# Performance work log

Hardware: AMD Instinct MI355X
Metric: run time of the kernel (lower is better)

Reference implementation:

```python
import jax, jax.numpy as jnp
import numpy as np

B, T, C = 8, 2048, 256
H = 4
HD = C // H  # 64

def setup_inputs() -> dict:
    key = jax.random.key(0)
    ks = jax.random.split(key, 5)
    s = 1.0 / np.sqrt(C)
    return {
        "x": jax.random.normal(ks[0], (B, T, C), dtype=jnp.float32),
        "w_qkv": jax.random.uniform(ks[1], (3 * C, C), jnp.float32, -s, s),
        "b_qkv": jax.random.uniform(ks[2], (3 * C,), jnp.float32, -s, s),
        "w_proj": jax.random.uniform(ks[3], (C, C), jnp.float32, -s, s),
        "b_proj": jax.random.uniform(ks[4], (C,), jnp.float32, -s, s),
    }

def reference(x, w_qkv, b_qkv, w_proj, b_proj):
    # qkv projection: [B,T,3C] -> [3,B,H,T,HD]
    qkv = x @ w_qkv.T + b_qkv
    qkv = qkv.reshape(B, T, 3, H, HD).transpose(2, 0, 3, 1, 4)
    q, k, v = qkv[0], qkv[1], qkv[2]
    scale = HD ** -0.5
    attn = jnp.einsum("bhqd,bhkd->bhqk", q, k) * scale
    attn = jax.nn.softmax(attn, axis=-1)  # dropout is identity in eval
    out = jnp.einsum("bhqk,bhkd->bhqd", attn, v)
    out = out.transpose(0, 2, 1, 3).reshape(B, T, C)
    return out @ w_proj.T + b_proj
```

## Files before the change

### kernel.cpp

```cpp
#include <hip/hip_runtime.h>
#include <hip/hip_bf16.h>
#include <cstdint>
#include <cstddef>


typedef __attribute__((ext_vector_type(8))) __bf16 bf16x8;
typedef __attribute__((ext_vector_type(4))) float f32x4;
typedef __attribute__((ext_vector_type(16))) float f32x16;

__device__ __forceinline__ f32x4 mfma16(bf16x8 a, bf16x8 b, f32x4 c) {
  return __builtin_amdgcn_mfma_f32_16x16x32_bf16(a, b, c, 0, 0, 0);
}
__device__ __forceinline__ f32x16 mfma32(bf16x8 a, bf16x8 b, f32x16 c) {
  return __builtin_amdgcn_mfma_f32_32x32x16_bf16(a, b, c, 0, 0, 0);
}

__device__ __forceinline__ void gload_lds16(const __bf16* g, __bf16* l) {
  __builtin_amdgcn_global_load_lds(
      (const __attribute__((address_space(1))) void*)g,
      (__attribute__((address_space(3))) void*)l, 16, 0, 0);
}

__device__ __forceinline__ uint32_t cvtpk_bf16(float lo, float hi) {
  uint32_t r;
  asm("v_cvt_pk_bf16_f32 %0, %1, %2" : "=v"(r) : "v"(lo), "v"(hi));
  return r;
}

__global__ __launch_bounds__(256) void cast_all(
    const float* __restrict__ x, const float* __restrict__ wq,
    const float* __restrict__ wp,
    __bf16* __restrict__ xb, __bf16* __restrict__ wqb, __bf16* __restrict__ wpb) {
  const int NX = (16384 * 256) / 4, NQ = (768 * 256) / 4, NP = (256 * 256) / 4;
  int i = blockIdx.x * 256 + threadIdx.x;
  const float4* src;
  __bf16* dst;
  int j;
  if (i < NX) { src = (const float4*)x; dst = xb; j = i; }
  else if (i < NX + NQ) { src = (const float4*)wq; dst = wqb; j = i - NX; }
  else if (i < NX + NQ + NP) { src = (const float4*)wp; dst = wpb; j = i - NX - NQ; }
  else return;
  float4 v = src[j];
  union { __bf16 b[4]; ushort4 u; } o;
  o.b[0] = (__bf16)v.x; o.b[1] = (__bf16)v.y; o.b[2] = (__bf16)v.z; o.b[3] = (__bf16)v.w;
  ((ushort4*)dst)[j] = o.u;
}

template <int EPI>
__global__ __launch_bounds__(256) void gemm_nt(
    const __bf16* __restrict__ A, const __bf16* __restrict__ B,
    const float* __restrict__ bias, int K, int N,
    __bf16* __restrict__ qo, __bf16* __restrict__ ko, __bf16* __restrict__ vo,
    float* __restrict__ fo) {
  const int tid = threadIdx.x;
  const int lane = tid & 63;
  const int w = tid >> 6;
  const int wr = w >> 1, wc = w & 1;
  const int m0 = blockIdx.x * 128, n0 = blockIdx.y * 128;
  const int l15 = lane & 15, lhi = lane >> 4;
  const bool vswap = (EPI == 0) && (n0 >= 512);

  __shared__ __align__(16) __bf16 As[128 * 64];
  __shared__ __align__(16) __bf16 Bs[128 * 64];

  const f32x4 fzero = {0.f, 0.f, 0.f, 0.f};
  f32x4 acc[4][4];
#pragma unroll
  for (int i = 0; i < 4; i++)
#pragma unroll
    for (int j = 0; j < 4; j++) acc[i][j] = fzero;

  for (int k0 = 0; k0 < K; k0 += 64) {
#pragma unroll
    for (int it = 0; it < 4; ++it) {
      int c = it * 256 + tid;
      int row = c >> 3, cc = c & 7;
      int col = ((cc ^ (row & 7)) << 3);
      gload_lds16(A + (size_t)(m0 + row) * K + k0 + col, As + c * 8);
      gload_lds16(B + (size_t)(n0 + row) * K + k0 + col, Bs + c * 8);
    }
    asm volatile("s_waitcnt vmcnt(0)" ::: "memory");
    __syncthreads();

    bf16x8 af[4][2], bfr[4][2];
#pragma unroll
    for (int i = 0; i < 4; i++)
#pragma unroll
      for (int kk = 0; kk < 2; kk++) {
        af[i][kk]  = *(const bf16x8*)(
            As + (wr * 64 + i * 16 + l15) * 64 + (((kk * 4 + lhi) ^ (l15 & 7)) << 3));
        bfr[i][kk] = *(const bf16x8*)(
            Bs + (wc * 64 + i * 16 + l15) * 64 + (((kk * 4 + lhi) ^ (l15 & 7)) << 3));
      }
    __builtin_amdgcn_s_setprio(1);
    if (!vswap) {
#pragma unroll
      for (int kk = 0; kk < 2; kk++)
#pragma unroll
        for (int mi = 0; mi < 4; mi++)
#pragma unroll
          for (int ni = 0; ni < 4; ni++)
            acc[mi][ni] = mfma16(af[mi][kk], bfr[ni][kk], acc[mi][ni]);
    } else {
#pragma unroll
      for (int kk = 0; kk < 2; kk++)
#pragma unroll
        for (int mi = 0; mi < 4; mi++)
#pragma unroll
          for (int ni = 0; ni < 4; ni++)
            acc[mi][ni] = mfma16(bfr[ni][kk], af[mi][kk], acc[mi][ni]);
    }
    __builtin_amdgcn_s_setprio(0);
    __syncthreads();
  }

  if (vswap) {
#pragma unroll
    for (int mi = 0; mi < 4; mi++) {
#pragma unroll
      for (int ni = 0; ni < 4; ni++) {
        int tg = m0 + wr * 64 + mi * 16 + l15;
        int nb = n0 + wc * 64 + ni * 16 + (lhi << 2);
        int b = tg >> 11, t = tg & 2047;
#pragma unroll
        for (int r = 0; r < 4; r++) {
          int n = nb + r;
          float val = acc[mi][ni][r] + bias[n];
          int hd = n - 512;
          int h = hd >> 6, d = hd & 63;
          vo[((size_t)(b * 4 + h) * 64 + d) * 2048 + t] = (__bf16)val;
        }
      }
    }
    return;
  }

#pragma unroll
  for (int mi = 0; mi < 4; mi++) {
#pragma unroll
    for (int ni = 0; ni < 4; ni++) {
      int col = n0 + wc * 64 + ni * 16 + l15;
      int rowb = m0 + wr * 64 + mi * 16 + (lhi << 2);
      float bv = bias[col];
#pragma unroll
      for (int r = 0; r < 4; r++) {
        float val = acc[mi][ni][r] + bv;
        int rr = rowb + r;
        if (EPI == 0) {
          int h = (col >> 6) & 3;
          int d = col & 63;
          int b = rr >> 11;
          int t = rr & 2047;
          size_t bh = (size_t)(b * 4 + h);
          if (col < 256) {
            qo[(bh * 2048 + t) * 64 + d] = (__bf16)(val * 0.18033688f);
          } else {
            ko[(bh * 2048 + t) * 64 + d] = (__bf16)val;
          }
        } else {
          fo[(size_t)rr * N + col] = val;
        }
      }
    }
  }
}

__global__ __launch_bounds__(256, 2) void attn_kernel(
    const __bf16* __restrict__ Q, const __bf16* __restrict__ Kb,
    const __bf16* __restrict__ Vt, __bf16* __restrict__ Ao) {
  const int tid = threadIdx.x, lane = tid & 63, w = tid >> 6;
  const int l31 = lane & 31, hi = lane >> 5;
  const int bh = blockIdx.y;
  const int q0 = blockIdx.x * 128;
  const int b = bh >> 2, h = bh & 3;

  __shared__ __align__(16) __bf16 Ks[2][64 * 64];
  __shared__ __align__(16) __bf16 Vs[2][64 * 64];
  __shared__ float Ls[4][32];

  const __bf16* Qb = Q + (size_t)bh * 2048 * 64;
  const __bf16* Kbase = Kb + (size_t)bh * 2048 * 64;
  const __bf16* Vbase = Vt + (size_t)bh * 64 * 2048;

  const int qrow = q0 + w * 32 + l31;
  bf16x8 qf[4];
#pragma unroll
  for (int dc = 0; dc < 4; dc++)
    qf[dc] = *(const bf16x8*)(Qb + (size_t)qrow * 64 + dc * 16 + hi * 8);

  f32x16 oacc[2];
#pragma unroll
  for (int i = 0; i < 16; i++) { oacc[0][i] = 0.f; oacc[1][i] = 0.f; }
  float lrun = 0.f;

  const int r0 = tid >> 3, p0c = tid & 7;
  const int s0 = ((p0c ^ (r0 & 7)) << 3);
  const int r1 = (tid + 256) >> 3, p1c = tid & 7;
  const int s1 = ((p1c ^ (r1 & 7)) << 3);

  gload_lds16(Kbase + (size_t)r0 * 64 + s0, &Ks[0][tid * 8]);
  gload_lds16(Kbase + (size_t)r1 * 64 + s1, &Ks[0][(tid + 256) * 8]);
  gload_lds16(Vbase + (size_t)r0 * 2048 + s0, &Vs[0][tid * 8]);
  gload_lds16(Vbase + (size_t)r1 * 2048 + s1, &Vs[0][(tid + 256) * 8]);

  int cur = 0;
  const int swz = (l31 & 7);

  for (int kt = 0; kt < 32; ++kt) {
    __syncthreads();

    if (kt + 1 < 32) {
      const __bf16* Kg = Kbase + (size_t)(kt + 1) * 64 * 64;
      const __bf16* Vg = Vbase + (size_t)(kt + 1) * 64;
      gload_lds16(Kg + (size_t)r0 * 64 + s0, &Ks[cur ^ 1][tid * 8]);
      gload_lds16(Kg + (size_t)r1 * 64 + s1, &Ks[cur ^ 1][(tid + 256) * 8]);
      gload_lds16(Vg + (size_t)r0 * 2048 + s0, &Vs[cur ^ 1][tid * 8]);
      gload_lds16(Vg + (size_t)r1 * 2048 + s1, &Vs[cur ^ 1][(tid + 256) * 8]);
    }

    const __bf16* Kl = &Ks[cur][0];
    const __bf16* Vl = &Vs[cur][0];

    f32x16 sacc[2];
#pragma unroll
    for (int i = 0; i < 16; i++) { sacc[0][i] = -16.f; sacc[1][i] = -16.f; }
#pragma unroll
    for (int kb = 0; kb < 2; kb++) {
      bf16x8 kf[4];
#pragma unroll
      for (int dc = 0; dc < 4; dc++)
        kf[dc] = *(const bf16x8*)(
            Kl + (kb * 32 + l31) * 64 + (((dc * 2 + hi) ^ swz) << 3));
      __builtin_amdgcn_s_setprio(1);
#pragma unroll
      for (int dc = 0; dc < 4; dc++)
        sacc[kb] = mfma32(kf[dc], qf[dc], sacc[kb]);
      __builtin_amdgcn_s_setprio(0);
    }

#pragma unroll
    for (int kb = 0; kb < 2; kb++)
#pragma unroll
      for (int i = 0; i < 16; i++) sacc[kb][i] = exp2f(sacc[kb][i]);

    uint32_t wo[8][2];
#pragma unroll
    for (int kb = 0; kb < 2; kb++)
#pragma unroll
      for (int e = 0; e < 4; e++) {
        wo[kb * 4 + e][0] = cvtpk_bf16(sacc[kb][4 * e + 0], sacc[kb][4 * e + 1]);
        wo[kb * 4 + e][1] = cvtpk_bf16(sacc[kb][4 * e + 2], sacc[kb][4 * e + 3]);
      }
    bf16x8 pa[4];
#pragma unroll
    for (int ks = 0; ks < 4; ks++) {
      uint32_t a0 = wo[2 * ks][0], b0 = wo[2 * ks + 1][0];
      uint32_t a1 = wo[2 * ks][1], b1 = wo[2 * ks + 1][1];
      asm("v_permlane32_swap_b32 %0, %1" : "+v"(a0), "+v"(b0));
      asm("v_permlane32_swap_b32 %0, %1" : "+v"(a1), "+v"(b1));
      union { uint32_t u[4]; bf16x8 v; } f;
      f.u[0] = a0; f.u[1] = a1; f.u[2] = b0; f.u[3] = b1;
      pa[ks] = f.v;
    }

    float red[16];
#pragma unroll
    for (int i = 0; i < 16; i++) red[i] = sacc[0][i] + sacc[1][i];
#pragma unroll
    for (int s = 8; s >= 1; s >>= 1)
#pragma unroll
      for (int i = 0; i < 8; i++)
        if (i < s) red[i] += red[i + s];
    lrun += red[0] + __shfl_xor(red[0], 32);

#pragma unroll
    for (int db = 0; db < 2; db++) {
      bf16x8 vf[4];
#pragma unroll
      for (int ks = 0; ks < 4; ks++)
        vf[ks] = *(const bf16x8*)(
            Vl + (db * 32 + l31) * 64 + (((ks * 2 + hi) ^ swz) << 3));
      __builtin_amdgcn_s_setprio(1);
#pragma unroll
      for (int ks = 0; ks < 4; ks++)
        oacc[db] = mfma32(pa[ks], vf[ks], oacc[db]);
      __builtin_amdgcn_s_setprio(0);
    }

    cur ^= 1;
  }

  if (hi == 0) Ls[w][l31] = lrun;
  asm volatile("s_waitcnt lgkmcnt(0)" ::: "memory");
  __builtin_amdgcn_sched_barrier(0);
  float linv[16];
#pragma unroll
  for (int r = 0; r < 16; r++)
    linv[r] = 1.0f / Ls[w][4 * hi + (r & 3) + 8 * (r >> 2)];
#pragma unroll
  for (int db = 0; db < 2; db++)
#pragma unroll
    for (int r = 0; r < 16; r++) {
      int qr = 4 * hi + (r & 3) + 8 * (r >> 2);
      int t = q0 + w * 32 + qr;
      Ao[((size_t)(b * 2048 + t)) * 256 + h * 64 + db * 32 + l31] =
          (__bf16)(oacc[db][r] * linv[r]);
    }
}

extern "C" void kernel_launch(void* const* d_in, const int* in_sizes, int n_in,
                              void* d_out, int out_size, void* d_ws, size_t ws_size,
                              hipStream_t stream) {
  const float* x      = (const float*)d_in[0];
  const float* w_qkv  = (const float*)d_in[1];
  const float* b_qkv  = (const float*)d_in[2];
  const float* w_proj = (const float*)d_in[3];
  const float* b_proj = (const float*)d_in[4];
  float* out = (float*)d_out;

  char* ws = (char*)d_ws;
  __bf16* xb  = (__bf16*)ws; ws += (size_t)16384 * 256 * 2;
  __bf16* wqb = (__bf16*)ws; ws += (size_t)768 * 256 * 2;
  __bf16* wpb = (__bf16*)ws; ws += (size_t)256 * 256 * 2;
  __bf16* qb  = (__bf16*)ws; ws += (size_t)8 * 4 * 2048 * 64 * 2;
  __bf16* kb  = (__bf16*)ws; ws += (size_t)8 * 4 * 2048 * 64 * 2;
  __bf16* vb  = (__bf16*)ws; ws += (size_t)8 * 4 * 2048 * 64 * 2;
  __bf16* aob = (__bf16*)ws; ws += (size_t)16384 * 256 * 2;

  int castN = (16384 * 256 + 768 * 256 + 256 * 256) / 4;
  cast_all<<<(castN + 255) / 256, 256, 0, stream>>>(x, w_qkv, w_proj, xb, wqb, wpb);
  gemm_nt<0><<<dim3(128, 6), 256, 0, stream>>>(xb, wqb, b_qkv, 256, 768,
                                               qb, kb, vb, nullptr);
  attn_kernel<<<dim3(16, 32), 256, 0, stream>>>(qb, kb, vb, aob);
  gemm_nt<1><<<dim3(128, 2), 256, 0, stream>>>(aob, wpb, b_proj, 256, 256,
                                               nullptr, nullptr, nullptr, out);
}
```

Before: 162.2 us.

## Split key sequence across two wave groups per attention block with LDS reduction

Doubles the attention block to 512 threads. Two groups of four waves each stream half of the key/value tiles into their own double-buffered LDS region. At the end, group 1 writes its partial output accumulators and row sums to shared memory, and group 0 adds them, normalises and stores the result. The partials can be added directly because the softmax uses a fixed offset rather than a running max. The aim is to halve each wave's serial key loop and raise waves per CU. The cost is a cross-group reduction through LDS, and the tighter launch bound (512, 4) may squeeze registers and cause spills.

New measurement: 233.4 us. 1.44x slower.

```diff
diff --git a/kernel.cpp b/kernel.cpp
--- a/kernel.cpp
+++ b/kernel.cpp
@@ -165,17 +165,20 @@
   }
 }
 
-__global__ __launch_bounds__(256, 2) void attn_kernel(
+__global__ __launch_bounds__(512, 4) void attn_kernel(
     const __bf16* __restrict__ Q, const __bf16* __restrict__ Kb,
     const __bf16* __restrict__ Vt, __bf16* __restrict__ Ao) {
-  const int tid = threadIdx.x, lane = tid & 63, w = tid >> 6;
+  const int tid = threadIdx.x, lane = tid & 63;
+  const int w8 = tid >> 6;
+  const int grp = w8 >> 2;
+  const int w = w8 & 3;
   const int l31 = lane & 31, hi = lane >> 5;
   const int bh = blockIdx.y;
   const int q0 = blockIdx.x * 128;
   const int b = bh >> 2, h = bh & 3;
 
-  __shared__ __align__(16) __bf16 Ks[2][64 * 64];
-  __shared__ __align__(16) __bf16 Vs[2][64 * 64];
+  __shared__ __align__(16) __bf16 KV[2][2][2][4096];
+  __shared__ float Lm[4][32];
   __shared__ float Ls[4][32];
 
   const __bf16* Qb = Q + (size_t)bh * 2048 * 64;
@@ -193,33 +196,42 @@
   for (int i = 0; i < 16; i++) { oacc[0][i] = 0.f; oacc[1][i] = 0.f; }
   float lrun = 0.f;
 
-  const int r0 = tid >> 3, p0c = tid & 7;
-  const int s0 = ((p0c ^ (r0 & 7)) << 3);
-  const int r1 = (tid + 256) >> 3, p1c = tid & 7;
-  const int s1 = ((p1c ^ (r1 & 7)) << 3);
-
-  gload_lds16(Kbase + (size_t)r0 * 64 + s0, &Ks[0][tid * 8]);
-  gload_lds16(Kbase + (size_t)r1 * 64 + s1, &Ks[0][(tid + 256) * 8]);
-  gload_lds16(Vbase + (size_t)r0 * 2048 + s0, &Vs[0][tid * 8]);
-  gload_lds16(Vbase + (size_t)r1 * 2048 + s1, &Vs[0][(tid + 256) * 8]);
+  const int tg = tid & 255;
+  const int r0 = tg >> 3, s0 = (((tg & 7) ^ (r0 & 7)) << 3);
+  const int r1 = r0 + 32, s1 = (((tg & 7) ^ (r1 & 7)) << 3);
+  const int kt0 = grp * 16;
+
+  __bf16* Kp = &KV[grp][0][0][0];
+  __bf16* Vp = &KV[grp][1][0][0];
+
+  {
+    const __bf16* Kg = Kbase + (size_t)kt0 * 64 * 64;
+    const __bf16* Vg = Vbase + (size_t)kt0 * 64;
+    gload_lds16(Kg + (size_t)r0 * 64 + s0, Kp + tg * 8);
+    gload_lds16(Kg + (size_t)r1 * 64 + s1, Kp + (tg + 256) * 8);
+    gload_lds16(Vg + (size_t)r0 * 2048 + s0, Vp + tg * 8);
+    gload_lds16(Vg + (size_t)r1 * 2048 + s1, Vp + (tg + 256) * 8);
+  }
 
   int cur = 0;
   const int swz = (l31 & 7);
 
-  for (int kt = 0; kt < 32; ++kt) {
+  for (int kt = 0; kt < 16; ++kt) {
     __syncthreads();
 
-    if (kt + 1 < 32) {
-      const __bf16* Kg = Kbase + (size_t)(kt + 1) * 64 * 64;
-      const __bf16* Vg = Vbase + (size_t)(kt + 1) * 64;
-      gload_lds16(Kg + (size_t)r0 * 64 + s0, &Ks[cur ^ 1][tid * 8]);
-      gload_lds16(Kg + (size_t)r1 * 64 + s1, &Ks[cur ^ 1][(tid + 256) * 8]);
-      gload_lds16(Vg + (size_t)r0 * 2048 + s0, &Vs[cur ^ 1][tid * 8]);
-      gload_lds16(Vg + (size_t)r1 * 2048 + s1, &Vs[cur ^ 1][(tid + 256) * 8]);
-    }
-
-    const __bf16* Kl = &Ks[cur][0];
-    const __bf16* Vl = &Vs[cur][0];
+    if (kt + 1 < 16) {
+      const __bf16* Kg = Kbase + (size_t)(kt0 + kt + 1) * 64 * 64;
+      const __bf16* Vg = Vbase + (size_t)(kt0 + kt + 1) * 64;
+      __bf16* Kd = Kp + (cur ^ 1) * 4096;
+      __bf16* Vd = Vp + (cur ^ 1) * 4096;
+      gload_lds16(Kg + (size_t)r0 * 64 + s0, Kd + tg * 8);
+      gload_lds16(Kg + (size_t)r1 * 64 + s1, Kd + (tg + 256) * 8);
+      gload_lds16(Vg + (size_t)r0 * 2048 + s0, Vd + tg * 8);
+      gload_lds16(Vg + (size_t)r1 * 2048 + s1, Vd + (tg + 256) * 8);
+    }
+
+    const __bf16* Kl = Kp + cur * 4096;
+    const __bf16* Vl = Vp + cur * 4096;
 
     f32x16 sacc[2];
 #pragma unroll
@@ -290,22 +302,45 @@
     cur ^= 1;
   }
 
-  if (hi == 0) Ls[w][l31] = lrun;
-  asm volatile("s_waitcnt lgkmcnt(0)" ::: "memory");
-  __builtin_amdgcn_sched_barrier(0);
-  float linv[16];
-#pragma unroll
-  for (int r = 0; r < 16; r++)
-    linv[r] = 1.0f / Ls[w][4 * hi + (r & 3) + 8 * (r >> 2)];
-#pragma unroll
-  for (int db = 0; db < 2; db++)
-#pragma unroll
-    for (int r = 0; r < 16; r++) {
-      int qr = 4 * hi + (r & 3) + 8 * (r >> 2);
-      int t = q0 + w * 32 + qr;
-      Ao[((size_t)(b * 2048 + t)) * 256 + h * 64 + db * 32 + l31] =
-          (__bf16)(oacc[db][r] * linv[r]);
-    }
+  __syncthreads();
+  float* Msh = (float*)&KV[0][0][0][0];
+
+  if (grp == 1) {
+    if (hi == 0) Lm[w][l31] = lrun;
+    int base = w * 64 + lane;
+#pragma unroll
+    for (int i = 0; i < 16; i++) {
+      Msh[(i * 2 + 0) * 256 + base] = oacc[0][i];
+      Msh[(i * 2 + 1) * 256 + base] = oacc[1][i];
+    }
+  }
+  __syncthreads();
+  if (grp == 0) {
+    lrun += Lm[w][l31];
+    int base = w * 64 + lane;
+#pragma unroll
+    for (int i = 0; i < 16; i++) {
+      oacc[0][i] += Msh[(i * 2 + 0) * 256 + base];
+      oacc[1][i] += Msh[(i * 2 + 1) * 256 + base];
+    }
+
+    if (hi == 0) Ls[w][l31] = lrun;
+    asm volatile("s_waitcnt lgkmcnt(0)" ::: "memory");
+    __builtin_amdgcn_sched_barrier(0);
+    float linv[16];
+#pragma unroll
+    for (int r = 0; r < 16; r++)
+      linv[r] = 1.0f / Ls[w][4 * hi + (r & 3) + 8 * (r >> 2)];
+#pragma unroll
+    for (int db = 0; db < 2; db++)
+#pragma unroll
+      for (int r = 0; r < 16; r++) {
+        int qr = 4 * hi + (r & 3) + 8 * (r >> 2);
+        int t = q0 + w * 32 + qr;
+        Ao[((size_t)(b * 2048 + t)) * 256 + h * 64 + db * 32 + l31] =
+            (__bf16)(oacc[db][r] * linv[r]);
+      }
+  }
 }
 
 extern "C" void kernel_launch(void* const* d_in, const int* in_sizes, int n_in,
@@ -331,7 +366,7 @@
   cast_all<<<(castN + 255) / 256, 256, 0, stream>>>(x, w_qkv, w_proj, xb, wqb, wpb);
   gemm_nt<0><<<dim3(128, 6), 256, 0, stream>>>(xb, wqb, b_qkv, 256, 768,
                                                qb, kb, vb, nullptr);
-  attn_kernel<<<dim3(16, 32), 256, 0, stream>>>(qb, kb, vb, aob);
+  attn_kernel<<<dim3(16, 32), 512, 0, stream>>>(qb, kb, vb, aob);
   gemm_nt<1><<<dim3(128, 2), 256, 0, stream>>>(aob, wpb, b_proj, 256, 256,
                                                nullptr, nullptr, nullptr, out);
 }
```
